# Kernel optimization log

Hardware: AMD Instinct MI355X
Metric: run time of the kernel (lower is better)

## Reference

```python
import jax, jax.numpy as jnp
import numpy as np

OUT, IN, RANK = 4096, 4096, 512
B, S = 4, 2048


def setup_inputs() -> dict:
    key = jax.random.key(0)
    k_x, k_qa, k_qb, k_sa, k_sb, k_b = jax.random.split(key, 6)
    x = jax.random.normal(k_x, (B, S, IN), dtype=jnp.float32)
    # int8-style symmetric quantized CP factors (stored as int32 for the harness)
    q_a = jax.random.randint(k_qa, (OUT, RANK), -127, 127, dtype=jnp.int32)
    q_b = jax.random.randint(k_qb, (IN, RANK), -127, 127, dtype=jnp.int32)
    scale_a = jax.random.uniform(k_sa, (), dtype=jnp.float32) * 0.01 + 1e-4
    scale_b = jax.random.uniform(k_sb, (), dtype=jnp.float32) * 0.01 + 1e-4
    bias = jax.random.normal(k_b, (OUT,), dtype=jnp.float32)
    return {"x": x, "q_a": q_a, "q_b": q_b, "scale_a": scale_a,
            "scale_b": scale_b, "bias": bias}


def reference(x, q_a, q_b, scale_a, scale_b, bias):
    # dequantize_factors(): symmetric per-factor dequant q * scale
    a = q_a.astype(jnp.float32) * scale_a          # [OUT, RANK]
    b = q_b.astype(jnp.float32) * scale_b          # [IN,  RANK]
    # CP reconstruction: weight = factors[0] @ factors[1].T, viewed as [OUT, IN]
    weight = a @ b.T                               # [OUT, IN] (materialized, as in original)
    # F.linear(x, weight, bias) = x @ weight.T + bias
    return jnp.einsum('bsi,oi->bso', x, weight) + bias
```

## Files before the change

kernel.cpp:

```cpp
#include <hip/hip_runtime.h>
#include <hip/hip_fp16.h>


#define M_TOT 8192
#define N_OUT 4096
#define K_IN  4096
#define RANK  512

typedef _Float16 f16x8 __attribute__((ext_vector_type(8)));
typedef float f32x4 __attribute__((ext_vector_type(4)));

#define WAIT_VM0() asm volatile("s_waitcnt vmcnt(0)" ::: "memory")
#define BARRIER() do { __builtin_amdgcn_s_barrier(); __builtin_amdgcn_sched_barrier(0); } while (0)

__device__ __forceinline__ void gload_lds16(const void* g, void* l) {
  __builtin_amdgcn_global_load_lds(
      (const __attribute__((address_space(1))) unsigned int*)g,
      (__attribute__((address_space(3))) unsigned int*)l, 16, 0, 0);
}

__global__ void k_cvt_qa(const int4* __restrict__ q, ushort4* __restrict__ o, int n4) {
  int i = blockIdx.x * blockDim.x + threadIdx.x;
  if (i >= n4) return;
  int4 v = q[i];
  ushort4 r;
  r.x = __half_as_ushort(__float2half_rn((float)v.x));
  r.y = __half_as_ushort(__float2half_rn((float)v.y));
  r.z = __half_as_ushort(__float2half_rn((float)v.z));
  r.w = __half_as_ushort(__float2half_rn((float)v.w));
  o[i] = r;
}

__global__ void k_transpose_qb(const int* __restrict__ qb, __half* __restrict__ qbt) {
  __shared__ __half tile[32][33];
  int tx = threadIdx.x & 31, ty = threadIdx.x >> 5;
  int k0 = blockIdx.x * 32, r0 = blockIdx.y * 32;
#pragma unroll
  for (int j = 0; j < 4; ++j)
    tile[ty + j * 8][tx] = __float2half_rn((float)qb[(size_t)(k0 + ty + j * 8) * RANK + r0 + tx]);
  __syncthreads();
#pragma unroll
  for (int j = 0; j < 4; ++j)
    qbt[(size_t)(r0 + ty + j * 8) * K_IN + k0 + tx] = tile[tx][ty + j * 8];
}

__global__ __launch_bounds__(512, 2) void k_gemm1v(
    const float* __restrict__ X, const __half* __restrict__ Bt,
    __half* __restrict__ P) {
  __shared__ __align__(16) uint4 lds[2][2048];
  const int tid = threadIdx.x;
  const int lane = tid & 63, wid = tid >> 6;
  const int wm = wid & 1, wn = wid >> 1;
  const int blk = blockIdx.x;
  const int xcd = blk & 7, m_t = blk >> 3;
  const int z = xcd >> 1, n_t = xcd & 1;
  const int m0 = m_t * 128, n0 = n_t * 256;
  const int kbeg = z * (K_IN / 4);
  const int fr = lane & 15, fq = lane >> 4;

  f32x4 acc[4][4] = {};

  auto stage = [&](int kt, int buf) {
#pragma unroll
    for (int c = 0; c < 2; ++c) {
      int d = tid + 512 * c;
      int r = d >> 3, s = (d & 7) ^ (r & 7);
      gload_lds16(X + (size_t)(m0 + r) * K_IN + kbeg + kt * 32 + s * 4, &lds[buf][d]);
    }
#pragma unroll
    for (int c = 0; c < 2; ++c) {
      int d = tid + 512 * c;
      int p = d >> 3, u = (d & 7) ^ (p & 7);
      gload_lds16(Bt + (size_t)(n0 + 2 * p + (u >> 2)) * K_IN + kbeg + kt * 32 + (u & 3) * 8,
                  &lds[buf][1024 + d]);
    }
  };

  stage(0, 0);
  WAIT_VM0();
  BARRIER();

  const int NT = (K_IN / 4) / 32;
  for (int t = 0; t < NT; ++t) {
    if (t + 1 < NT) stage(t + 1, (t + 1) & 1);
    const uint4* Ab = &lds[t & 1][0];
    const uint4* Bb = &lds[t & 1][1024];
    f16x8 a[4], b[4];
#pragma unroll
    for (int mi = 0; mi < 4; ++mi) {
      int r = wm * 64 + mi * 16 + fr;
      f32x4 u0 = *(const f32x4*)&Ab[r * 8 + ((fq * 2) ^ (r & 7))];
      f32x4 u1 = *(const f32x4*)&Ab[r * 8 + ((fq * 2 + 1) ^ (r & 7))];
      union { __half2 h[4]; f16x8 v; } pa;
      pa.h[0] = __floats2half2_rn(u0[0], u0[1]);
      pa.h[1] = __floats2half2_rn(u0[2], u0[3]);
      pa.h[2] = __floats2half2_rn(u1[0], u1[1]);
      pa.h[3] = __floats2half2_rn(u1[2], u1[3]);
      a[mi] = pa.v;
    }
#pragma unroll
    for (int ni = 0; ni < 4; ++ni) {
      int r = wn * 64 + ni * 16 + fr;
      int p = r >> 1;
      b[ni] = *(const f16x8*)&Bb[p * 8 + ((((r & 1) << 2) | fq) ^ (p & 7))];
    }
#pragma unroll
    for (int mi = 0; mi < 4; ++mi)
#pragma unroll
      for (int ni = 0; ni < 4; ++ni)
        acc[mi][ni] = __builtin_amdgcn_mfma_f32_16x16x32_f16(a[mi], b[ni], acc[mi][ni], 0, 0, 0);

    if (t + 1 < NT) WAIT_VM0();
    BARRIER();
  }

  __half* Pz = P + (size_t)z * M_TOT * RANK;
#pragma unroll
  for (int mi = 0; mi < 4; ++mi)
#pragma unroll
    for (int ni = 0; ni < 4; ++ni) {
      int col = n0 + wn * 64 + ni * 16 + fr;
      int rbase = m0 + wm * 64 + mi * 16 + fq * 4;
#pragma unroll
      for (int j = 0; j < 4; ++j)
        Pz[(size_t)(rbase + j) * RANK + col] = __float2half_rn(acc[mi][ni][j]);
    }
}

__global__ void k_reduce_t(const uint4* __restrict__ P, uint4* __restrict__ T8, int n8) {
  int i = blockIdx.x * blockDim.x + threadIdx.x;
  if (i >= n8) return;
  float2 f[4] = {};
#pragma unroll
  for (int zz = 0; zz < 4; ++zz) {
    uint4 v = P[(size_t)zz * n8 + i];
    const __half2* h = (const __half2*)&v;
#pragma unroll
    for (int j = 0; j < 4; ++j) {
      float2 g = __half22float2(h[j]);
      f[j].x += g.x; f[j].y += g.y;
    }
  }
  uint4 r;
  __half2* o = (__half2*)&r;
#pragma unroll
  for (int j = 0; j < 4; ++j) o[j] = __floats2half2_rn(f[j].x, f[j].y);
  T8[i] = r;
}

__global__ __launch_bounds__(256, 2) void k_gemm2(
    const __half* __restrict__ T, const __half* __restrict__ QA,
    const float* __restrict__ sa, const float* __restrict__ sb,
    const float* __restrict__ bias, float* __restrict__ Out) {
  __shared__ __align__(16) uint4 lds[2][2048];
  const int tid = threadIdx.x;
  const int lane = tid & 63, wid = tid >> 6, wm = wid & 1, wn = wid >> 1;
  const int flat = blockIdx.x;
  const int xcd = flat & 7, local = flat >> 3;
  const int n_t = xcd * 4 + (local & 3);
  const int m_t = local >> 2;
  const int m0 = m_t * 128, n0 = n_t * 128;
  const int fr = lane & 15, fq = lane >> 4;

  f32x4 acc[4][4] = {};

  auto stage = [&](int kt, int buf) {
#pragma unroll
    for (int c = 0; c < 4; ++c) {
      int d = tid + 256 * c;
      int r = d >> 3, s = (d & 7) ^ (r & 7);
      gload_lds16(T + (size_t)(m0 + r) * RANK + kt * 64 + s * 8, &lds[buf][d]);
    }
#pragma unroll
    for (int c = 0; c < 4; ++c) {
      int d = tid + 256 * c;
      int r = d >> 3, s = (d & 7) ^ (r & 7);
      gload_lds16(QA + (size_t)(n0 + r) * RANK + kt * 64 + s * 8, &lds[buf][1024 + d]);
    }
  };

  stage(0, 0);
  WAIT_VM0();
  BARRIER();

  const int NT = RANK / 64;
  for (int t = 0; t < NT; ++t) {
    if (t + 1 < NT) stage(t + 1, (t + 1) & 1);
    const int cur = t & 1;
#pragma unroll
    for (int kk = 0; kk < 2; ++kk) {
      int s = kk * 4 + fq;
      f16x8 a[4], b[4];
#pragma unroll
      for (int mi = 0; mi < 4; ++mi) {
        int r = wm * 64 + mi * 16 + fr;
        a[mi] = *(const f16x8*)&lds[cur][r * 8 + (s ^ (r & 7))];
      }
#pragma unroll
      for (int ni = 0; ni < 4; ++ni) {
        int n = wn * 64 + ni * 16 + fr;
        b[ni] = *(const f16x8*)&lds[cur][1024 + n * 8 + (s ^ (n & 7))];
      }
#pragma unroll
      for (int mi = 0; mi < 4; ++mi)
#pragma unroll
        for (int ni = 0; ni < 4; ++ni)
          acc[mi][ni] = __builtin_amdgcn_mfma_f32_16x16x32_f16(a[mi], b[ni], acc[mi][ni], 0, 0, 0);
    }
    if (t + 1 < NT) WAIT_VM0();
    BARRIER();
  }

  const float scale = sa[0] * sb[0];
#pragma unroll
  for (int mi = 0; mi < 4; ++mi)
#pragma unroll
    for (int ni = 0; ni < 4; ++ni) {
      int col = n0 + wn * 64 + ni * 16 + fr;
      float bv = bias[col];
      int rbase = m0 + wm * 64 + mi * 16 + fq * 4;
#pragma unroll
      for (int j = 0; j < 4; ++j)
        Out[(size_t)(rbase + j) * N_OUT + col] = acc[mi][ni][j] * scale + bv;
    }
}

extern "C" void kernel_launch(void* const* d_in, const int* in_sizes, int n_in,
                              void* d_out, int out_size, void* d_ws, size_t ws_size,
                              hipStream_t stream) {
  const float* x    = (const float*)d_in[0];
  const int*   qa   = (const int*)d_in[1];
  const int*   qb   = (const int*)d_in[2];
  const float* sa   = (const float*)d_in[3];
  const float* sb   = (const float*)d_in[4];
  const float* bias = (const float*)d_in[5];
  float* out = (float*)d_out;

  char* ws = (char*)d_ws;
  __half* qa_h = (__half*)ws;
  __half* qbt  = (__half*)(ws + (4u << 20));
  __half* t    = (__half*)(ws + (8u << 20));
  __half* part = (__half*)(ws + (16u << 20));

  k_cvt_qa<<<2048, 256, 0, stream>>>((const int4*)qa, (ushort4*)qa_h, (N_OUT * RANK) / 4);
  dim3 tg(K_IN / 32, RANK / 32);
  k_transpose_qb<<<tg, 256, 0, stream>>>(qb, qbt);

  k_gemm1v<<<512, 512, 0, stream>>>(x, qbt, part);

  const int n8 = M_TOT * RANK / 8;
  k_reduce_t<<<n8 / 256, 256, 0, stream>>>((const uint4*)part, (uint4*)t, n8);

  k_gemm2<<<2048, 256, 0, stream>>>(t, qa_h, sa, sb, bias, out);
}
```

Before: 149.4 us.

## Load X directly to registers in GEMM1 and deepen LDS prefetch to two stages

GEMM1 now reads the fp32 X tile straight from global memory into registers instead of staging it through LDS. Only the B tile stays in LDS, which halves LDS use and raises the occupancy hint to 4 blocks per CU. Both GEMMs now prefetch two K-tiles ahead using partial vmcnt waits instead of draining all loads each iteration, aiming to hide global-load latency. The direct X loads are no longer swizzled or shared through LDS, so each wave issues its own strided global reads and the vmcnt accounting has to track these extra loads correctly.

```diff
diff --git a/kernel.cpp b/kernel.cpp
--- a/kernel.cpp
+++ b/kernel.cpp
@@ -11,6 +11,8 @@
 typedef float f32x4 __attribute__((ext_vector_type(4)));
 
 #define WAIT_VM0() asm volatile("s_waitcnt vmcnt(0)" ::: "memory")
+#define WAIT_VM2() asm volatile("s_waitcnt vmcnt(2)" ::: "memory")
+#define WAIT_VM8() asm volatile("s_waitcnt vmcnt(8)" ::: "memory")
 #define BARRIER() do { __builtin_amdgcn_s_barrier(); __builtin_amdgcn_sched_barrier(0); } while (0)
 
 __device__ __forceinline__ void gload_lds16(const void* g, void* l) {
@@ -44,10 +46,10 @@
     qbt[(size_t)(r0 + ty + j * 8) * K_IN + k0 + tx] = tile[tx][ty + j * 8];
 }
 
-__global__ __launch_bounds__(512, 2) void k_gemm1v(
+__global__ __launch_bounds__(512, 4) void k_gemm1r(
     const float* __restrict__ X, const __half* __restrict__ Bt,
     __half* __restrict__ P) {
-  __shared__ __align__(16) uint4 lds[2][2048];
+  __shared__ __align__(16) uint4 lds[2][1024];
   const int tid = threadIdx.x;
   const int lane = tid & 63, wid = tid >> 6;
   const int wm = wid & 1, wn = wid >> 1;
@@ -60,37 +62,31 @@
 
   f32x4 acc[4][4] = {};
 
-  auto stage = [&](int kt, int buf) {
-#pragma unroll
-    for (int c = 0; c < 2; ++c) {
-      int d = tid + 512 * c;
-      int r = d >> 3, s = (d & 7) ^ (r & 7);
-      gload_lds16(X + (size_t)(m0 + r) * K_IN + kbeg + kt * 32 + s * 4, &lds[buf][d]);
-    }
+  const float* abase = X + (size_t)(m0 + wm * 64 + fr) * K_IN + kbeg + fq * 8;
+
+  auto stageB = [&](int kt, int buf) {
 #pragma unroll
     for (int c = 0; c < 2; ++c) {
       int d = tid + 512 * c;
       int p = d >> 3, u = (d & 7) ^ (p & 7);
       gload_lds16(Bt + (size_t)(n0 + 2 * p + (u >> 2)) * K_IN + kbeg + kt * 32 + (u & 3) * 8,
-                  &lds[buf][1024 + d]);
+                  &lds[buf][d]);
     }
   };
 
-  stage(0, 0);
-  WAIT_VM0();
+  stageB(0, 0);
+  stageB(1, 1);
+  WAIT_VM2();
   BARRIER();
 
   const int NT = (K_IN / 4) / 32;
   for (int t = 0; t < NT; ++t) {
-    if (t + 1 < NT) stage(t + 1, (t + 1) & 1);
-    const uint4* Ab = &lds[t & 1][0];
-    const uint4* Bb = &lds[t & 1][1024];
-    f16x8 a[4], b[4];
+    f16x8 a[4];
 #pragma unroll
     for (int mi = 0; mi < 4; ++mi) {
-      int r = wm * 64 + mi * 16 + fr;
-      f32x4 u0 = *(const f32x4*)&Ab[r * 8 + ((fq * 2) ^ (r & 7))];
-      f32x4 u1 = *(const f32x4*)&Ab[r * 8 + ((fq * 2 + 1) ^ (r & 7))];
+      const float* p = abase + (size_t)mi * 16 * K_IN + t * 32;
+      f32x4 u0 = *(const f32x4*)p;
+      f32x4 u1 = *(const f32x4*)(p + 4);
       union { __half2 h[4]; f16x8 v; } pa;
       pa.h[0] = __floats2half2_rn(u0[0], u0[1]);
       pa.h[1] = __floats2half2_rn(u0[2], u0[3]);
@@ -98,6 +94,8 @@
       pa.h[3] = __floats2half2_rn(u1[2], u1[3]);
       a[mi] = pa.v;
     }
+    const uint4* Bb = &lds[t & 1][0];
+    f16x8 b[4];
 #pragma unroll
     for (int ni = 0; ni < 4; ++ni) {
       int r = wn * 64 + ni * 16 + fr;
@@ -110,7 +108,14 @@
       for (int ni = 0; ni < 4; ++ni)
         acc[mi][ni] = __builtin_amdgcn_mfma_f32_16x16x32_f16(a[mi], b[ni], acc[mi][ni], 0, 0, 0);
 
-    if (t + 1 < NT) WAIT_VM0();
+    if (t == NT - 1) break;
+    BARRIER();
+    if (t + 2 < NT) {
+      stageB(t + 2, t & 1);
+      WAIT_VM2();
+    } else {
+      WAIT_VM0();
+    }
     BARRIER();
   }
 
@@ -180,12 +185,12 @@
   };
 
   stage(0, 0);
-  WAIT_VM0();
+  stage(1, 1);
+  WAIT_VM8();
   BARRIER();
 
   const int NT = RANK / 64;
   for (int t = 0; t < NT; ++t) {
-    if (t + 1 < NT) stage(t + 1, (t + 1) & 1);
     const int cur = t & 1;
 #pragma unroll
     for (int kk = 0; kk < 2; ++kk) {
@@ -207,7 +212,14 @@
         for (int ni = 0; ni < 4; ++ni)
           acc[mi][ni] = __builtin_amdgcn_mfma_f32_16x16x32_f16(a[mi], b[ni], acc[mi][ni], 0, 0, 0);
     }
-    if (t + 1 < NT) WAIT_VM0();
+    if (t == NT - 1) break;
+    BARRIER();
+    if (t + 2 < NT) {
+      stage(t + 2, cur);
+      WAIT_VM8();
+    } else {
+      WAIT_VM0();
+    }
     BARRIER();
   }
 
@@ -246,7 +258,7 @@
   dim3 tg(K_IN / 32, RANK / 32);
   k_transpose_qb<<<tg, 256, 0, stream>>>(qb, qbt);
 
-  k_gemm1v<<<512, 512, 0, stream>>>(x, qbt, part);
+  k_gemm1r<<<512, 512, 0, stream>>>(x, qbt, part);
 
   const int n8 = M_TOT * RANK / 8;
   k_reduce_t<<<n8 / 256, 256, 0, stream>>>((const uint4*)part, (uint4*)t, n8);
```

New measurement: 222.1 us. +48.7%, slower.

## Deepen load pipeline to two stages ahead and widen gemm2 tiles to 128x256

Applied to the files above, without the earlier changes.

Both GEMM kernels now issue global-to-LDS loads two K-steps ahead. They wait with partial vmcnt counts so the next tile's loads stay in flight during compute, instead of draining all loads every iteration. gemm2 is restructured to 512-thread blocks covering 128x256 output tiles with a K-step of 32, which halves the grid and reuses each T tile across more columns. gemm1's launch bounds are raised to 4 blocks per CU. The extra barrier per iteration and the tighter register budget could offset the overlap gains.

```diff
diff --git a/kernel.cpp b/kernel.cpp
--- a/kernel.cpp
+++ b/kernel.cpp
@@ -11,6 +11,8 @@
 typedef float f32x4 __attribute__((ext_vector_type(4)));
 
 #define WAIT_VM0() asm volatile("s_waitcnt vmcnt(0)" ::: "memory")
+#define WAIT_VM3() asm volatile("s_waitcnt vmcnt(3)" ::: "memory")
+#define WAIT_VM4() asm volatile("s_waitcnt vmcnt(4)" ::: "memory")
 #define BARRIER() do { __builtin_amdgcn_s_barrier(); __builtin_amdgcn_sched_barrier(0); } while (0)
 
 __device__ __forceinline__ void gload_lds16(const void* g, void* l) {
@@ -44,7 +46,7 @@
     qbt[(size_t)(r0 + ty + j * 8) * K_IN + k0 + tx] = tile[tx][ty + j * 8];
 }
 
-__global__ __launch_bounds__(512, 2) void k_gemm1v(
+__global__ __launch_bounds__(512, 4) void k_gemm1v(
     const float* __restrict__ X, const __half* __restrict__ Bt,
     __half* __restrict__ P) {
   __shared__ __align__(16) uint4 lds[2][2048];
@@ -77,12 +79,12 @@
   };
 
   stage(0, 0);
-  WAIT_VM0();
+  stage(1, 1);
+  WAIT_VM4();
   BARRIER();
 
   const int NT = (K_IN / 4) / 32;
   for (int t = 0; t < NT; ++t) {
-    if (t + 1 < NT) stage(t + 1, (t + 1) & 1);
     const uint4* Ab = &lds[t & 1][0];
     const uint4* Bb = &lds[t & 1][1024];
     f16x8 a[4], b[4];
@@ -110,7 +112,14 @@
       for (int ni = 0; ni < 4; ++ni)
         acc[mi][ni] = __builtin_amdgcn_mfma_f32_16x16x32_f16(a[mi], b[ni], acc[mi][ni], 0, 0, 0);
 
-    if (t + 1 < NT) WAIT_VM0();
+    if (t == NT - 1) break;
+    BARRIER();
+    if (t + 2 < NT) {
+      stage(t + 2, t & 1);
+      WAIT_VM4();
+    } else {
+      WAIT_VM0();
+    }
     BARRIER();
   }
 
@@ -148,66 +157,71 @@
   T8[i] = r;
 }
 
-__global__ __launch_bounds__(256, 2) void k_gemm2(
+__global__ __launch_bounds__(512, 2) void k_gemm2w(
     const __half* __restrict__ T, const __half* __restrict__ QA,
     const float* __restrict__ sa, const float* __restrict__ sb,
     const float* __restrict__ bias, float* __restrict__ Out) {
-  __shared__ __align__(16) uint4 lds[2][2048];
+  __shared__ __align__(16) uint4 lds[2][1536];
   const int tid = threadIdx.x;
-  const int lane = tid & 63, wid = tid >> 6, wm = wid & 1, wn = wid >> 1;
-  const int flat = blockIdx.x;
-  const int xcd = flat & 7, local = flat >> 3;
-  const int n_t = xcd * 4 + (local & 3);
-  const int m_t = local >> 2;
-  const int m0 = m_t * 128, n0 = n_t * 128;
+  const int lane = tid & 63, wid = tid >> 6;
+  const int wm = wid & 1, wn = wid >> 1;
+  const int blk = blockIdx.x;
+  const int xcd = blk & 7, local = blk >> 3;
+  const int n_t = xcd * 2 + (local & 1);
+  const int m_t = local >> 1;
+  const int m0 = m_t * 128, n0 = n_t * 256;
   const int fr = lane & 15, fq = lane >> 4;
 
   f32x4 acc[4][4] = {};
 
   auto stage = [&](int kt, int buf) {
-#pragma unroll
-    for (int c = 0; c < 4; ++c) {
-      int d = tid + 256 * c;
-      int r = d >> 3, s = (d & 7) ^ (r & 7);
-      gload_lds16(T + (size_t)(m0 + r) * RANK + kt * 64 + s * 8, &lds[buf][d]);
-    }
-#pragma unroll
-    for (int c = 0; c < 4; ++c) {
-      int d = tid + 256 * c;
-      int r = d >> 3, s = (d & 7) ^ (r & 7);
-      gload_lds16(QA + (size_t)(n0 + r) * RANK + kt * 64 + s * 8, &lds[buf][1024 + d]);
+    {
+      int d = tid;
+      int r = d >> 2, s = (d & 3) ^ (r & 3);
+      gload_lds16(T + (size_t)(m0 + r) * RANK + kt * 32 + s * 8, &lds[buf][d]);
+    }
+#pragma unroll
+    for (int c = 0; c < 2; ++c) {
+      int d = tid + 512 * c;
+      int r = d >> 2, s = (d & 3) ^ (r & 3);
+      gload_lds16(QA + (size_t)(n0 + r) * RANK + kt * 32 + s * 8, &lds[buf][512 + d]);
     }
   };
 
   stage(0, 0);
-  WAIT_VM0();
+  stage(1, 1);
+  WAIT_VM3();
   BARRIER();
 
-  const int NT = RANK / 64;
+  const int NT = RANK / 32;
   for (int t = 0; t < NT; ++t) {
-    if (t + 1 < NT) stage(t + 1, (t + 1) & 1);
-    const int cur = t & 1;
-#pragma unroll
-    for (int kk = 0; kk < 2; ++kk) {
-      int s = kk * 4 + fq;
-      f16x8 a[4], b[4];
-#pragma unroll
-      for (int mi = 0; mi < 4; ++mi) {
-        int r = wm * 64 + mi * 16 + fr;
-        a[mi] = *(const f16x8*)&lds[cur][r * 8 + (s ^ (r & 7))];
-      }
-#pragma unroll
-      for (int ni = 0; ni < 4; ++ni) {
-        int n = wn * 64 + ni * 16 + fr;
-        b[ni] = *(const f16x8*)&lds[cur][1024 + n * 8 + (s ^ (n & 7))];
-      }
-#pragma unroll
-      for (int mi = 0; mi < 4; ++mi)
-#pragma unroll
-        for (int ni = 0; ni < 4; ++ni)
-          acc[mi][ni] = __builtin_amdgcn_mfma_f32_16x16x32_f16(a[mi], b[ni], acc[mi][ni], 0, 0, 0);
-    }
-    if (t + 1 < NT) WAIT_VM0();
+    const uint4* Ab = &lds[t & 1][0];
+    const uint4* Bb = &lds[t & 1][512];
+    f16x8 a[4], b[4];
+#pragma unroll
+    for (int mi = 0; mi < 4; ++mi) {
+      int r = wm * 64 + mi * 16 + fr;
+      a[mi] = *(const f16x8*)&Ab[r * 4 + (fq ^ (r & 3))];
+    }
+#pragma unroll
+    for (int ni = 0; ni < 4; ++ni) {
+      int n = wn * 64 + ni * 16 + fr;
+      b[ni] = *(const f16x8*)&Bb[n * 4 + (fq ^ (n & 3))];
+    }
+#pragma unroll
+    for (int mi = 0; mi < 4; ++mi)
+#pragma unroll
+      for (int ni = 0; ni < 4; ++ni)
+        acc[mi][ni] = __builtin_amdgcn_mfma_f32_16x16x32_f16(a[mi], b[ni], acc[mi][ni], 0, 0, 0);
+
+    if (t == NT - 1) break;
+    BARRIER();
+    if (t + 2 < NT) {
+      stage(t + 2, t & 1);
+      WAIT_VM3();
+    } else {
+      WAIT_VM0();
+    }
     BARRIER();
   }
 
@@ -251,5 +265,5 @@
   const int n8 = M_TOT * RANK / 8;
   k_reduce_t<<<n8 / 256, 256, 0, stream>>>((const uint4*)part, (uint4*)t, n8);
 
-  k_gemm2<<<2048, 256, 0, stream>>>(t, qa_h, sa, sb, bias, out);
-}
+  k_gemm2w<<<1024, 512, 0, stream>>>(t, qa_h, sa, sb, bias, out);
+}
```

New measurement: 143.3 us. 1.04x faster.

## Single-buffer GEMM1 with split-K 8 and higher occupancy; deepen GEMM2 prefetch

Applied to the files above, without the earlier changes.

GEMM1 drops LDS double buffering for a single buffer with plain syncthreads, and raises launch bounds to 4 blocks per CU so several blocks hide latency instead of in-kernel prefetch. It also adds a split-K=8 variant with 1024 blocks, chosen when the workspace is large enough, which doubles the partial-sum traffic through the reduction kernel. GEMM2 now prefetches two stages ahead and waits with a partial vmcnt count. The risks are load latency that is no longer overlapped within a block and the extra partial-buffer reads and writes.

```diff
diff --git a/kernel.cpp b/kernel.cpp
--- a/kernel.cpp
+++ b/kernel.cpp
@@ -11,6 +11,7 @@
 typedef float f32x4 __attribute__((ext_vector_type(4)));
 
 #define WAIT_VM0() asm volatile("s_waitcnt vmcnt(0)" ::: "memory")
+#define WAIT_VM8() asm volatile("s_waitcnt vmcnt(8)" ::: "memory")
 #define BARRIER() do { __builtin_amdgcn_s_barrier(); __builtin_amdgcn_sched_barrier(0); } while (0)
 
 __device__ __forceinline__ void gload_lds16(const void* g, void* l) {
@@ -44,53 +45,52 @@
     qbt[(size_t)(r0 + ty + j * 8) * K_IN + k0 + tx] = tile[tx][ty + j * 8];
 }
 
-__global__ __launch_bounds__(512, 2) void k_gemm1v(
+template <int SK>
+__global__ __launch_bounds__(512, 4) void k_gemm1s(
     const float* __restrict__ X, const __half* __restrict__ Bt,
     __half* __restrict__ P) {
-  __shared__ __align__(16) uint4 lds[2][2048];
+  __shared__ __align__(16) uint4 lds[2048];
   const int tid = threadIdx.x;
   const int lane = tid & 63, wid = tid >> 6;
   const int wm = wid & 1, wn = wid >> 1;
   const int blk = blockIdx.x;
-  const int xcd = blk & 7, m_t = blk >> 3;
-  const int z = xcd >> 1, n_t = xcd & 1;
+  const int xcd = blk & 7, local = blk >> 3;
+  int z, n_t, m_t;
+  if constexpr (SK == 8) {
+    int combo = xcd * 2 + (local & 1);
+    z = combo >> 1; n_t = combo & 1; m_t = local >> 1;
+  } else {
+    z = xcd >> 1; n_t = xcd & 1; m_t = local;
+  }
   const int m0 = m_t * 128, n0 = n_t * 256;
-  const int kbeg = z * (K_IN / 4);
+  const int kbeg = z * (K_IN / SK);
   const int fr = lane & 15, fq = lane >> 4;
 
   f32x4 acc[4][4] = {};
 
-  auto stage = [&](int kt, int buf) {
+  const int NT = (K_IN / SK) / 32;
+  for (int t = 0; t < NT; ++t) {
+    const int k0 = kbeg + t * 32;
 #pragma unroll
     for (int c = 0; c < 2; ++c) {
       int d = tid + 512 * c;
       int r = d >> 3, s = (d & 7) ^ (r & 7);
-      gload_lds16(X + (size_t)(m0 + r) * K_IN + kbeg + kt * 32 + s * 4, &lds[buf][d]);
+      gload_lds16(X + (size_t)(m0 + r) * K_IN + k0 + s * 4, &lds[d]);
     }
 #pragma unroll
     for (int c = 0; c < 2; ++c) {
       int d = tid + 512 * c;
       int p = d >> 3, u = (d & 7) ^ (p & 7);
-      gload_lds16(Bt + (size_t)(n0 + 2 * p + (u >> 2)) * K_IN + kbeg + kt * 32 + (u & 3) * 8,
-                  &lds[buf][1024 + d]);
-    }
-  };
-
-  stage(0, 0);
-  WAIT_VM0();
-  BARRIER();
-
-  const int NT = (K_IN / 4) / 32;
-  for (int t = 0; t < NT; ++t) {
-    if (t + 1 < NT) stage(t + 1, (t + 1) & 1);
-    const uint4* Ab = &lds[t & 1][0];
-    const uint4* Bb = &lds[t & 1][1024];
+      gload_lds16(Bt + (size_t)(n0 + 2 * p + (u >> 2)) * K_IN + k0 + (u & 3) * 8,
+                  &lds[1024 + d]);
+    }
+    __syncthreads();
     f16x8 a[4], b[4];
 #pragma unroll
     for (int mi = 0; mi < 4; ++mi) {
       int r = wm * 64 + mi * 16 + fr;
-      f32x4 u0 = *(const f32x4*)&Ab[r * 8 + ((fq * 2) ^ (r & 7))];
-      f32x4 u1 = *(const f32x4*)&Ab[r * 8 + ((fq * 2 + 1) ^ (r & 7))];
+      f32x4 u0 = *(const f32x4*)&lds[r * 8 + ((fq * 2) ^ (r & 7))];
+      f32x4 u1 = *(const f32x4*)&lds[r * 8 + ((fq * 2 + 1) ^ (r & 7))];
       union { __half2 h[4]; f16x8 v; } pa;
       pa.h[0] = __floats2half2_rn(u0[0], u0[1]);
       pa.h[1] = __floats2half2_rn(u0[2], u0[3]);
@@ -102,16 +102,14 @@
     for (int ni = 0; ni < 4; ++ni) {
       int r = wn * 64 + ni * 16 + fr;
       int p = r >> 1;
-      b[ni] = *(const f16x8*)&Bb[p * 8 + ((((r & 1) << 2) | fq) ^ (p & 7))];
+      b[ni] = *(const f16x8*)&lds[1024 + p * 8 + ((((r & 1) << 2) | fq) ^ (p & 7))];
     }
 #pragma unroll
     for (int mi = 0; mi < 4; ++mi)
 #pragma unroll
       for (int ni = 0; ni < 4; ++ni)
         acc[mi][ni] = __builtin_amdgcn_mfma_f32_16x16x32_f16(a[mi], b[ni], acc[mi][ni], 0, 0, 0);
-
-    if (t + 1 < NT) WAIT_VM0();
-    BARRIER();
+    __syncthreads();
   }
 
   __half* Pz = P + (size_t)z * M_TOT * RANK;
@@ -127,12 +125,13 @@
     }
 }
 
+template <int SK>
 __global__ void k_reduce_t(const uint4* __restrict__ P, uint4* __restrict__ T8, int n8) {
   int i = blockIdx.x * blockDim.x + threadIdx.x;
   if (i >= n8) return;
   float2 f[4] = {};
 #pragma unroll
-  for (int zz = 0; zz < 4; ++zz) {
+  for (int zz = 0; zz < SK; ++zz) {
     uint4 v = P[(size_t)zz * n8 + i];
     const __half2* h = (const __half2*)&v;
 #pragma unroll
@@ -180,12 +179,12 @@
   };
 
   stage(0, 0);
-  WAIT_VM0();
+  stage(1, 1);
+  WAIT_VM8();
   BARRIER();
 
   const int NT = RANK / 64;
   for (int t = 0; t < NT; ++t) {
-    if (t + 1 < NT) stage(t + 1, (t + 1) & 1);
     const int cur = t & 1;
 #pragma unroll
     for (int kk = 0; kk < 2; ++kk) {
@@ -207,7 +206,14 @@
         for (int ni = 0; ni < 4; ++ni)
           acc[mi][ni] = __builtin_amdgcn_mfma_f32_16x16x32_f16(a[mi], b[ni], acc[mi][ni], 0, 0, 0);
     }
-    if (t + 1 < NT) WAIT_VM0();
+    if (t == NT - 1) break;
+    BARRIER();
+    if (t + 2 < NT) {
+      stage(t + 2, cur);
+      WAIT_VM8();
+    } else {
+      WAIT_VM0();
+    }
     BARRIER();
   }
 
@@ -246,10 +252,14 @@
   dim3 tg(K_IN / 32, RANK / 32);
   k_transpose_qb<<<tg, 256, 0, stream>>>(qb, qbt);
 
-  k_gemm1v<<<512, 512, 0, stream>>>(x, qbt, part);
-
   const int n8 = M_TOT * RANK / 8;
-  k_reduce_t<<<n8 / 256, 256, 0, stream>>>((const uint4*)part, (uint4*)t, n8);
+  if (ws_size >= (80ull << 20)) {
+    k_gemm1s<8><<<1024, 512, 0, stream>>>(x, qbt, part);
+    k_reduce_t<8><<<n8 / 256, 256, 0, stream>>>((const uint4*)part, (uint4*)t, n8);
+  } else {
+    k_gemm1s<4><<<512, 512, 0, stream>>>(x, qbt, part);
+    k_reduce_t<4><<<n8 / 256, 256, 0, stream>>>((const uint4*)part, (uint4*)t, n8);
+  }
 
   k_gemm2<<<2048, 256, 0, stream>>>(t, qa_h, sa, sb, bias, out);
 }
```

After: 144.7 us. 3.1% less time.
